# Kernel optimization log

Measured on AMD Instinct MI355X. Metric: run time of the kernel, lower is better.

The kernel has to match this reference:

```python
import jax, jax.numpy as jnp
import numpy as np

C1 = 384  # input channel dim (hardcoded in source)


def setup_inputs() -> dict:
    key = jax.random.key(0)
    kx, kq, kk, kv = jax.random.split(key, 4)
    B, T, C, H = 512, 256, C1, 64
    x = jax.random.normal(kx, (B, T, C), dtype=jnp.float32)
    # nn.Linear(C1, head_size, bias=False) weights, stored as (C, H) for x @ W
    Wq = jax.random.normal(kq, (C, H), dtype=jnp.float32) * (1.0 / np.sqrt(C))
    Wk = jax.random.normal(kk, (C, H), dtype=jnp.float32) * (1.0 / np.sqrt(C))
    Wv = jax.random.normal(kv, (C, H), dtype=jnp.float32) * (1.0 / np.sqrt(C))
    return {"x": x, "Wq": Wq, "Wk": Wk, "Wv": Wv}


def reference(x, Wq, Wk, Wv):
    B, T, C = x.shape
    q = jnp.einsum('btc,ch->bth', x, Wq)  # [B,T,H]
    k = jnp.einsum('btc,ch->bth', x, Wk)
    v = jnp.einsum('btc,ch->bth', x, Wv)
    # NOTE: source MULTIPLIES by C**0.5 (not the usual 1/sqrt(d)) -- faithful.
    scale = jnp.asarray(C, x.dtype) ** 0.5
    wei = jnp.einsum('bth,bsh->bts', q, k) * scale  # [B,T,T]
    causal = jnp.tril(jnp.ones((T, T), dtype=bool))
    wei = jnp.where(causal, wei, -jnp.inf)
    wei = jax.nn.softmax(wei, axis=-1)
    # dropout is identity in eval mode (deterministic reference)
    out = jnp.einsum('bts,bsh->bth', wei, v)  # [B,T,H]
    return out
```

## Files before the change

kernel.cpp:

```cpp
#include <hip/hip_runtime.h>
#include <hip/hip_bf16.h>
#include <math.h>

typedef _Float16 f16x8 __attribute__((ext_vector_type(8)));
typedef _Float16 f16x4 __attribute__((ext_vector_type(4)));
typedef float f32x4 __attribute__((ext_vector_type(4)));

#define MFMA16(a, b, c) __builtin_amdgcn_mfma_f32_16x16x32_f16((a), (b), (c), 0, 0, 0)

typedef __attribute__((address_space(3))) char as3_char;
typedef __attribute__((address_space(1))) const char as1_char;
__device__ __forceinline__ void glds16(const void* g, void* l) {
  __builtin_amdgcn_global_load_lds((as1_char*)g, (as3_char*)l, 16, 0, 0);
}

__global__ __launch_bounds__(256) void wprep_kernel(
    const float* __restrict__ Wq, const float* __restrict__ Wk, const float* __restrict__ Wv,
    _Float16* __restrict__ wstg) {
  int s = blockIdx.x * 256 + threadIdx.x;
  int c0 = s / 1536, s2 = s % 1536;
  int p = s2 / 768, r = (s2 % 768) / 4, gg = s2 & 3;
  int g = gg ^ ((r >> 1) & 3);
  int sel = r >> 6, h = r & 63;
  const float* W = (sel == 0) ? Wq : (sel == 1) ? Wk : Wv;
  f16x8 o;
#pragma unroll
  for (int e = 0; e < 8; ++e) {
    float val = W[(c0 * 32 + g * 8 + e) * 64 + h];
    _Float16 hi = (_Float16)val;
    o[e] = p ? (_Float16)(val - (float)hi) : hi;
  }
  *(f16x8*)&wstg[(size_t)s * 8] = o;
}

__global__ __launch_bounds__(512, 2) void fused_kernel(
    const float* __restrict__ x,
    const _Float16* __restrict__ wstg,
    float* __restrict__ out) {
  __shared__ __align__(16) char smem[156672];
  _Float16* kh = (_Float16*)smem;
  _Float16* kl = (_Float16*)(smem + 36864);
  _Float16* vT = (_Float16*)(smem + 73728);
  char* wbuf0 = smem + 107520;
  char* wbuf1 = smem + 132096;
  _Float16* slc = (_Float16*)(smem + 107520);

  const int tid = threadIdx.x;
  const int wave = tid >> 6, lane = tid & 63;
  const int g = lane >> 4, l16 = lane & 15;
  const int b = blockIdx.x;
  const int rset[2] = {16 * wave, 240 - 16 * wave};
  const float* xb = x + (size_t)b * 98304;
  _Float16* wsl = slc + wave * 2304;

  const float K2 = 28.270933f;
  const float NINF = -__builtin_inff();

  const float* xrow0 = xb + (size_t)(rset[0] + l16) * 384 + g * 8;
  const float* xrow1 = xb + (size_t)(rset[1] + l16) * 384 + g * 8;

  f32x4 qa[2][4] = {}, ka[2][4] = {}, va[2][4] = {};
  float4 buf[3][2][2];

#pragma unroll
  for (int i = 0; i < 3; ++i) {
    int seg0 = wave * 192 + i * 64;
    glds16(wstg + (size_t)(seg0 + lane) * 8, wbuf0 + seg0 * 16);
  }
  __builtin_amdgcn_sched_barrier(0);
#pragma unroll
  for (int p = 0; p < 2; ++p) {
    buf[p][0][0] = *(const float4*)(xrow0 + p * 32);
    buf[p][0][1] = *(const float4*)(xrow0 + p * 32 + 4);
    buf[p][1][0] = *(const float4*)(xrow1 + p * 32);
    buf[p][1][1] = *(const float4*)(xrow1 + p * 32 + 4);
  }
  __builtin_amdgcn_sched_barrier(0);
  asm volatile("s_waitcnt vmcnt(4) lgkmcnt(0)" ::: "memory");
  __builtin_amdgcn_s_barrier();
  __builtin_amdgcn_sched_barrier(0);

#pragma unroll
  for (int c = 0; c < 12; ++c) {
    if (c < 11) {
      char* nb = ((c + 1) & 1) ? wbuf1 : wbuf0;
      const _Float16* src = wstg + (size_t)(c + 1) * 12288;
#pragma unroll
      for (int i = 0; i < 3; ++i) {
        int seg0 = wave * 192 + i * 64;
        glds16(src + (size_t)(seg0 + lane) * 8, nb + seg0 * 16);
      }
    }
    __builtin_amdgcn_sched_barrier(0);
    if (c < 10) {
      buf[(c + 2) % 3][0][0] = *(const float4*)(xrow0 + (c + 2) * 32);
      buf[(c + 2) % 3][0][1] = *(const float4*)(xrow0 + (c + 2) * 32 + 4);
      buf[(c + 2) % 3][1][0] = *(const float4*)(xrow1 + (c + 2) * 32);
      buf[(c + 2) % 3][1][1] = *(const float4*)(xrow1 + (c + 2) * 32 + 4);
    }
    __builtin_amdgcn_sched_barrier(0);

    const char* wb = (c & 1) ? wbuf1 : wbuf0;
    f16x8 ah[2], al[2];
#pragma unroll
    for (int s = 0; s < 2; ++s) {
      float vv[8] = {buf[c % 3][s][0].x, buf[c % 3][s][0].y, buf[c % 3][s][0].z,
                     buf[c % 3][s][0].w, buf[c % 3][s][1].x, buf[c % 3][s][1].y,
                     buf[c % 3][s][1].z, buf[c % 3][s][1].w};
#pragma unroll
      for (int e = 0; e < 8; ++e) {
        _Float16 h = (_Float16)vv[e];
        ah[s][e] = h;
        al[s][e] = (_Float16)(vv[e] - (float)h);
      }
    }
#pragma unroll
    for (int ct = 0; ct < 4; ++ct) {
      const int rq = ct * 16 + l16;
      const int rk = 64 + ct * 16 + l16;
      const int rv = 128 + ct * 16 + l16;
      f16x8 bqh = *(const f16x8*)(wb + (0 * 768 + rq * 4 + (g ^ ((rq >> 1) & 3))) * 16);
      f16x8 bql = *(const f16x8*)(wb + (1 * 768 + rq * 4 + (g ^ ((rq >> 1) & 3))) * 16);
      f16x8 bkh = *(const f16x8*)(wb + (0 * 768 + rk * 4 + (g ^ ((rk >> 1) & 3))) * 16);
      f16x8 bkl = *(const f16x8*)(wb + (1 * 768 + rk * 4 + (g ^ ((rk >> 1) & 3))) * 16);
      f16x8 bvh = *(const f16x8*)(wb + (0 * 768 + rv * 4 + (g ^ ((rv >> 1) & 3))) * 16);
#pragma unroll
      for (int s = 0; s < 2; ++s) {
        qa[s][ct] = MFMA16(ah[s], bqh, qa[s][ct]);
        qa[s][ct] = MFMA16(al[s], bqh, qa[s][ct]);
        qa[s][ct] = MFMA16(ah[s], bql, qa[s][ct]);
        ka[s][ct] = MFMA16(ah[s], bkh, ka[s][ct]);
        ka[s][ct] = MFMA16(al[s], bkh, ka[s][ct]);
        ka[s][ct] = MFMA16(ah[s], bkl, ka[s][ct]);
        va[s][ct] = MFMA16(ah[s], bvh, va[s][ct]);
      }
    }
    if (c < 10) {
      asm volatile("s_waitcnt vmcnt(4) lgkmcnt(0)" ::: "memory");
    } else if (c == 10) {
      asm volatile("s_waitcnt vmcnt(0) lgkmcnt(0)" ::: "memory");
    } else {
      asm volatile("s_waitcnt lgkmcnt(0)" ::: "memory");
    }
    __builtin_amdgcn_s_barrier();
    __builtin_amdgcn_sched_barrier(0);
  }

#pragma unroll
  for (int s = 0; s < 2; ++s) {
    const int rs = rset[s];
#pragma unroll
    for (int ct = 0; ct < 4; ++ct) {
      const int h = ct * 16 + l16;
#pragma unroll
      for (int j = 0; j < 4; ++j) {
        const int row = rs + 4 * g + j;
        float kv = ka[s][ct][j];
        _Float16 khv = (_Float16)kv;
        kh[row * 72 + h] = khv;
        kl[row * 72 + h] = (_Float16)(kv - (float)khv);
        vT[h * 264 + row] = (_Float16)va[s][ct][j];
      }
    }
  }
  __syncthreads();

  f16x8 qhf[2][2], qlf[2][2];
#pragma unroll
  for (int ct = 0; ct < 4; ++ct) {
    const int h = ct * 16 + l16;
#pragma unroll
    for (int j = 0; j < 4; ++j) {
      const int rl = 4 * g + j;
      float qv = qa[0][ct][j];
      _Float16 qh = (_Float16)qv;
      wsl[(rl * 2 + 0) * 72 + h] = qh;
      wsl[(rl * 2 + 1) * 72 + h] = (_Float16)(qv - (float)qh);
    }
  }
  __syncthreads();
#pragma unroll
  for (int ks = 0; ks < 2; ++ks) {
    qhf[0][ks] = *(const f16x8*)&wsl[(l16 * 2 + 0) * 72 + ks * 32 + g * 8];
    qlf[0][ks] = *(const f16x8*)&wsl[(l16 * 2 + 1) * 72 + ks * 32 + g * 8];
  }
  __syncthreads();
#pragma unroll
  for (int ct = 0; ct < 4; ++ct) {
    const int h = ct * 16 + l16;
#pragma unroll
    for (int j = 0; j < 4; ++j) {
      const int rl = 4 * g + j;
      float qv = qa[1][ct][j];
      _Float16 qh = (_Float16)qv;
      wsl[(rl * 2 + 0) * 72 + h] = qh;
      wsl[(rl * 2 + 1) * 72 + h] = (_Float16)(qv - (float)qh);
    }
  }
  __syncthreads();
#pragma unroll
  for (int ks = 0; ks < 2; ++ks) {
    qhf[1][ks] = *(const f16x8*)&wsl[(l16 * 2 + 0) * 72 + ks * 32 + g * 8];
    qlf[1][ks] = *(const f16x8*)&wsl[(l16 * 2 + 1) * 72 + ks * 32 + g * 8];
  }
  asm volatile("s_waitcnt lgkmcnt(0)" ::: "memory");
  __builtin_amdgcn_sched_barrier(0);

  _Float16* psl = wsl;
  float mrun[2] = {NINF, NINF}, srun[2] = {0.f, 0.f};
  f32x4 O[2][4] = {};

  for (int c = 0; c < 4; ++c) {
    const int kb = c * 64;
#pragma unroll
    for (int s = 0; s < 2; ++s) {
      const int rs = rset[s];
      if (kb > rs + 15) continue;
      const int qr = rs + l16;
      f32x4 sa[4] = {};
#pragma unroll
      for (int kt = 0; kt < 4; ++kt) {
        if (kb + 16 * kt > rs + 15) continue;
#pragma unroll
        for (int ks = 0; ks < 2; ++ks) {
          const int ko = (kb + 16 * kt + l16) * 72 + ks * 32 + g * 8;
          f16x8 akh = *(const f16x8*)&kh[ko];
          f16x8 akl = *(const f16x8*)&kl[ko];
          sa[kt] = MFMA16(akh, qhf[s][ks], sa[kt]);
          sa[kt] = MFMA16(akl, qhf[s][ks], sa[kt]);
          sa[kt] = MFMA16(akh, qlf[s][ks], sa[kt]);
        }
      }
      float cm = NINF;
#pragma unroll
      for (int kt = 0; kt < 4; ++kt)
#pragma unroll
        for (int j = 0; j < 4; ++j) {
          const int krow = kb + 16 * kt + 4 * g + j;
          float sv = (krow <= qr) ? sa[kt][j] : NINF;
          sa[kt][j] = sv;
          cm = fmaxf(cm, sv);
        }
      cm = fmaxf(cm, __shfl_xor(cm, 16));
      cm = fmaxf(cm, __shfl_xor(cm, 32));
      const float mn = fmaxf(mrun[s], cm);
      const float scl = exp2f(K2 * (mrun[s] - mn));
      mrun[s] = mn;
      float cs = 0.f;
#pragma unroll
      for (int kt = 0; kt < 4; ++kt)
#pragma unroll
        for (int j = 0; j < 4; ++j) {
          float p = exp2f(K2 * (sa[kt][j] - mn));
          cs += p;
          psl[(s * 16 + l16) * 72 + kt * 16 + 4 * g + j] = (_Float16)p;
        }
      cs += __shfl_xor(cs, 16);
      cs += __shfl_xor(cs, 32);
      srun[s] = srun[s] * scl + cs;
#pragma unroll
      for (int ht = 0; ht < 4; ++ht) O[s][ht] *= scl;
      asm volatile("s_waitcnt lgkmcnt(0)" ::: "memory");
      __builtin_amdgcn_sched_barrier(0);
#pragma unroll
      for (int ks2 = 0; ks2 < 2; ++ks2) {
        f16x8 bp = *(const f16x8*)&psl[(s * 16 + l16) * 72 + ks2 * 32 + g * 8];
#pragma unroll
        for (int ht = 0; ht < 4; ++ht) {
          f16x8 av = *(const f16x8*)&vT[(ht * 16 + l16) * 264 + kb + ks2 * 32 + g * 8];
          O[s][ht] = MFMA16(av, bp, O[s][ht]);
        }
      }
    }
  }

#pragma unroll
  for (int s = 0; s < 2; ++s) {
    const int qr = rset[s] + l16;
    const float inv = 1.0f / srun[s];
#pragma unroll
    for (int ht = 0; ht < 4; ++ht) {
      f32x4 r = O[s][ht] * inv;
      *(f32x4*)&out[((size_t)b * 256 + qr) * 64 + ht * 16 + 4 * g] = r;
    }
  }
}

extern "C" void kernel_launch(void* const* d_in, const int* in_sizes, int n_in,
                              void* d_out, int out_size, void* d_ws, size_t ws_size,
                              hipStream_t stream) {
  const float* x  = (const float*)d_in[0];
  const float* Wq = (const float*)d_in[1];
  const float* Wk = (const float*)d_in[2];
  const float* Wv = (const float*)d_in[3];

  _Float16* wstg = (_Float16*)d_ws;

  wprep_kernel<<<72, 256, 0, stream>>>(Wq, Wk, Wv, wstg);
  fused_kernel<<<512, 512, 0, stream>>>(x, wstg, (float*)d_out);
}
```

Measured before the change: 86.00 us.

## Fuse both query row-sets per key chunk, use packed f16 converts and setprio

The attention loop now processes both 16-row query sets together inside each key chunk. Each K and V fragment loaded from LDS is reused for two MFMA chains, and the two softmax updates run before a single shared PV stage. The hi/lo fp16 split of x uses packed round-toward-zero conversions (cvt_pkrtz) in place of per-element casts. s_setprio is raised around MFMA bursts. This cuts LDS reads and exposes more independent MFMA work, at the cost of more live registers and a rounding mode change on the high part, which the low-part residual compensates for.

```diff
diff --git a/kernel.cpp b/kernel.cpp
--- a/kernel.cpp
+++ b/kernel.cpp
@@ -4,6 +4,8 @@
 
 typedef _Float16 f16x8 __attribute__((ext_vector_type(8)));
 typedef _Float16 f16x4 __attribute__((ext_vector_type(4)));
+typedef _Float16 f16x2 __attribute__((ext_vector_type(2)));
+typedef __fp16 fp16x2 __attribute__((ext_vector_type(2)));
 typedef float f32x4 __attribute__((ext_vector_type(4)));
 
 #define MFMA16(a, b, c) __builtin_amdgcn_mfma_f32_16x16x32_f16((a), (b), (c), 0, 0, 0)
@@ -12,6 +14,13 @@
 typedef __attribute__((address_space(1))) const char as1_char;
 __device__ __forceinline__ void glds16(const void* g, void* l) {
   __builtin_amdgcn_global_load_lds((as1_char*)g, (as3_char*)l, 16, 0, 0);
+}
+
+union F16x8u { f16x8 v; f16x2 h[4]; };
+
+__device__ __forceinline__ f16x2 pkrtz(float a, float b) {
+  fp16x2 r = __builtin_amdgcn_cvt_pkrtz(a, b);
+  return __builtin_bit_cast(f16x2, r);
 }
 
 __global__ __launch_bounds__(256) void wprep_kernel(
@@ -107,12 +116,16 @@
       float vv[8] = {buf[c % 3][s][0].x, buf[c % 3][s][0].y, buf[c % 3][s][0].z,
                      buf[c % 3][s][0].w, buf[c % 3][s][1].x, buf[c % 3][s][1].y,
                      buf[c % 3][s][1].z, buf[c % 3][s][1].w};
-#pragma unroll
-      for (int e = 0; e < 8; ++e) {
-        _Float16 h = (_Float16)vv[e];
-        ah[s][e] = h;
-        al[s][e] = (_Float16)(vv[e] - (float)h);
-      }
+      F16x8u uh, ul;
+#pragma unroll
+      for (int k2 = 0; k2 < 4; ++k2) {
+        float a = vv[2 * k2], bb = vv[2 * k2 + 1];
+        f16x2 hp = pkrtz(a, bb);
+        uh.h[k2] = hp;
+        ul.h[k2] = pkrtz(a - (float)hp[0], bb - (float)hp[1]);
+      }
+      ah[s] = uh.v;
+      al[s] = ul.v;
     }
 #pragma unroll
     for (int ct = 0; ct < 4; ++ct) {
@@ -124,6 +137,7 @@
       f16x8 bkh = *(const f16x8*)(wb + (0 * 768 + rk * 4 + (g ^ ((rk >> 1) & 3))) * 16);
       f16x8 bkl = *(const f16x8*)(wb + (1 * 768 + rk * 4 + (g ^ ((rk >> 1) & 3))) * 16);
       f16x8 bvh = *(const f16x8*)(wb + (0 * 768 + rv * 4 + (g ^ ((rv >> 1) & 3))) * 16);
+      __builtin_amdgcn_s_setprio(1);
 #pragma unroll
       for (int s = 0; s < 2; ++s) {
         qa[s][ct] = MFMA16(ah[s], bqh, qa[s][ct]);
@@ -134,6 +148,7 @@
         ka[s][ct] = MFMA16(ah[s], bkl, ka[s][ct]);
         va[s][ct] = MFMA16(ah[s], bvh, va[s][ct]);
       }
+      __builtin_amdgcn_s_setprio(0);
     }
     if (c < 10) {
       asm volatile("s_waitcnt vmcnt(4) lgkmcnt(0)" ::: "memory");
@@ -209,67 +224,116 @@
   _Float16* psl = wsl;
   float mrun[2] = {NINF, NINF}, srun[2] = {0.f, 0.f};
   f32x4 O[2][4] = {};
+  const int rs0 = rset[0], rs1 = rset[1];
+  const int qr0 = rs0 + l16, qr1 = rs1 + l16;
 
   for (int c = 0; c < 4; ++c) {
     const int kb = c * 64;
-#pragma unroll
-    for (int s = 0; s < 2; ++s) {
-      const int rs = rset[s];
-      if (kb > rs + 15) continue;
-      const int qr = rs + l16;
-      f32x4 sa[4] = {};
-#pragma unroll
-      for (int kt = 0; kt < 4; ++kt) {
-        if (kb + 16 * kt > rs + 15) continue;
-#pragma unroll
-        for (int ks = 0; ks < 2; ++ks) {
-          const int ko = (kb + 16 * kt + l16) * 72 + ks * 32 + g * 8;
-          f16x8 akh = *(const f16x8*)&kh[ko];
-          f16x8 akl = *(const f16x8*)&kl[ko];
-          sa[kt] = MFMA16(akh, qhf[s][ks], sa[kt]);
-          sa[kt] = MFMA16(akl, qhf[s][ks], sa[kt]);
-          sa[kt] = MFMA16(akh, qlf[s][ks], sa[kt]);
-        }
-      }
+    const bool a0 = (kb <= rs0 + 15);
+    const bool a1 = (kb <= rs1 + 15);
+    if (!a0 && !a1) continue;
+    f32x4 s0[4] = {}, s1[4] = {};
+#pragma unroll
+    for (int kt = 0; kt < 4; ++kt) {
+      const int kr = kb + 16 * kt;
+      const bool t0 = a0 && (kr <= rs0 + 15);
+      const bool t1 = a1 && (kr <= rs1 + 15);
+      if (!t0 && !t1) continue;
+#pragma unroll
+      for (int ks = 0; ks < 2; ++ks) {
+        const int ko = (kr + l16) * 72 + ks * 32 + g * 8;
+        f16x8 akh = *(const f16x8*)&kh[ko];
+        f16x8 akl = *(const f16x8*)&kl[ko];
+        __builtin_amdgcn_s_setprio(1);
+        if (t0) {
+          s0[kt] = MFMA16(akh, qhf[0][ks], s0[kt]);
+          s0[kt] = MFMA16(akl, qhf[0][ks], s0[kt]);
+          s0[kt] = MFMA16(akh, qlf[0][ks], s0[kt]);
+        }
+        if (t1) {
+          s1[kt] = MFMA16(akh, qhf[1][ks], s1[kt]);
+          s1[kt] = MFMA16(akl, qhf[1][ks], s1[kt]);
+          s1[kt] = MFMA16(akh, qlf[1][ks], s1[kt]);
+        }
+        __builtin_amdgcn_s_setprio(0);
+      }
+    }
+    if (a0) {
       float cm = NINF;
 #pragma unroll
       for (int kt = 0; kt < 4; ++kt)
 #pragma unroll
         for (int j = 0; j < 4; ++j) {
           const int krow = kb + 16 * kt + 4 * g + j;
-          float sv = (krow <= qr) ? sa[kt][j] : NINF;
-          sa[kt][j] = sv;
+          float sv = (krow <= qr0) ? s0[kt][j] : NINF;
+          s0[kt][j] = sv;
           cm = fmaxf(cm, sv);
         }
       cm = fmaxf(cm, __shfl_xor(cm, 16));
       cm = fmaxf(cm, __shfl_xor(cm, 32));
-      const float mn = fmaxf(mrun[s], cm);
-      const float scl = exp2f(K2 * (mrun[s] - mn));
-      mrun[s] = mn;
+      const float mn = fmaxf(mrun[0], cm);
+      const float scl = exp2f(K2 * (mrun[0] - mn));
+      mrun[0] = mn;
       float cs = 0.f;
 #pragma unroll
       for (int kt = 0; kt < 4; ++kt)
 #pragma unroll
         for (int j = 0; j < 4; ++j) {
-          float p = exp2f(K2 * (sa[kt][j] - mn));
+          float p = exp2f(K2 * (s0[kt][j] - mn));
           cs += p;
-          psl[(s * 16 + l16) * 72 + kt * 16 + 4 * g + j] = (_Float16)p;
+          psl[l16 * 72 + kt * 16 + 4 * g + j] = (_Float16)p;
         }
       cs += __shfl_xor(cs, 16);
       cs += __shfl_xor(cs, 32);
-      srun[s] = srun[s] * scl + cs;
-#pragma unroll
-      for (int ht = 0; ht < 4; ++ht) O[s][ht] *= scl;
-      asm volatile("s_waitcnt lgkmcnt(0)" ::: "memory");
-      __builtin_amdgcn_sched_barrier(0);
-#pragma unroll
-      for (int ks2 = 0; ks2 < 2; ++ks2) {
-        f16x8 bp = *(const f16x8*)&psl[(s * 16 + l16) * 72 + ks2 * 32 + g * 8];
-#pragma unroll
-        for (int ht = 0; ht < 4; ++ht) {
-          f16x8 av = *(const f16x8*)&vT[(ht * 16 + l16) * 264 + kb + ks2 * 32 + g * 8];
-          O[s][ht] = MFMA16(av, bp, O[s][ht]);
-        }
+      srun[0] = srun[0] * scl + cs;
+#pragma unroll
+      for (int ht = 0; ht < 4; ++ht) O[0][ht] *= scl;
+    }
+    if (a1) {
+      float cm = NINF;
+#pragma unroll
+      for (int kt = 0; kt < 4; ++kt)
+#pragma unroll
+        for (int j = 0; j < 4; ++j) {
+          const int krow = kb + 16 * kt + 4 * g + j;
+          float sv = (krow <= qr1) ? s1[kt][j] : NINF;
+          s1[kt][j] = sv;
+          cm = fmaxf(cm, sv);
+        }
+      cm = fmaxf(cm, __shfl_xor(cm, 16));
+      cm = fmaxf(cm, __shfl_xor(cm, 32));
+      const float mn = fmaxf(mrun[1], cm);
+      const float scl = exp2f(K2 * (mrun[1] - mn));
+      mrun[1] = mn;
+      float cs = 0.f;
+#pragma unroll
+      for (int kt = 0; kt < 4; ++kt)
+#pragma unroll
+        for (int j = 0; j < 4; ++j) {
+          float p = exp2f(K2 * (s1[kt][j] - mn));
+          cs += p;
+          psl[(16 + l16) * 72 + kt * 16 + 4 * g + j] = (_Float16)p;
+        }
+      cs += __shfl_xor(cs, 16);
+      cs += __shfl_xor(cs, 32);
+      srun[1] = srun[1] * scl + cs;
+#pragma unroll
+      for (int ht = 0; ht < 4; ++ht) O[1][ht] *= scl;
+    }
+    asm volatile("s_waitcnt lgkmcnt(0)" ::: "memory");
+    __builtin_amdgcn_sched_barrier(0);
+#pragma unroll
+    for (int ks2 = 0; ks2 < 2; ++ks2) {
+      f16x8 bp0 = {}, bp1 = {};
+      if (a0) bp0 = *(const f16x8*)&psl[l16 * 72 + ks2 * 32 + g * 8];
+      if (a1) bp1 = *(const f16x8*)&psl[(16 + l16) * 72 + ks2 * 32 + g * 8];
+#pragma unroll
+      for (int ht = 0; ht < 4; ++ht) {
+        f16x8 av = *(const f16x8*)&vT[(ht * 16 + l16) * 264 + kb + ks2 * 32 + g * 8];
+        __builtin_amdgcn_s_setprio(1);
+        if (a0) O[0][ht] = MFMA16(av, bp0, O[0][ht]);
+        if (a1) O[1][ht] = MFMA16(av, bp1, O[1][ht]);
+        __builtin_amdgcn_s_setprio(0);
       }
     }
   }
```

After: 83.63 us. 1.03x faster.

## Use 16 waves per block with one 16-row query tile per wave

Applied to the files above, without the earlier changes.

The fused attention kernel moves from 8 waves, each owning two row tiles (a low and a mirrored high tile for causal balance), to 16 waves per block, each owning one 16-row tile. The aim is to double the waves available per block for latency hiding. Only 12 waves issue weight loads into LDS, Q staging is done in two rounds, and MFMA sections are wrapped in s_setprio. Conversion to fp16 hi/lo now uses packed cvt_pkrtz, which rounds toward zero and can shift precision slightly. Costs: the causal load balance from paired tiles is lost, so later waves do much more work than early ones, and register pressure under launch bounds of 1024 may force spills.

```diff
diff --git a/kernel.cpp b/kernel.cpp
--- a/kernel.cpp
+++ b/kernel.cpp
@@ -4,6 +4,8 @@
 
 typedef _Float16 f16x8 __attribute__((ext_vector_type(8)));
 typedef _Float16 f16x4 __attribute__((ext_vector_type(4)));
+typedef _Float16 f16x2 __attribute__((ext_vector_type(2)));
+typedef __fp16 fp16x2 __attribute__((ext_vector_type(2)));
 typedef float f32x4 __attribute__((ext_vector_type(4)));
 
 #define MFMA16(a, b, c) __builtin_amdgcn_mfma_f32_16x16x32_f16((a), (b), (c), 0, 0, 0)
@@ -12,6 +14,13 @@
 typedef __attribute__((address_space(1))) const char as1_char;
 __device__ __forceinline__ void glds16(const void* g, void* l) {
   __builtin_amdgcn_global_load_lds((as1_char*)g, (as3_char*)l, 16, 0, 0);
+}
+
+union F16x8u { f16x8 v; f16x2 h[4]; };
+
+__device__ __forceinline__ f16x2 pkrtz(float a, float b) {
+  fp16x2 r = __builtin_amdgcn_cvt_pkrtz(a, b);
+  return __builtin_bit_cast(f16x2, r);
 }
 
 __global__ __launch_bounds__(256) void wprep_kernel(
@@ -33,7 +42,7 @@
   *(f16x8*)&wstg[(size_t)s * 8] = o;
 }
 
-__global__ __launch_bounds__(512, 2) void fused_kernel(
+__global__ __launch_bounds__(1024) void fused_kernel(
     const float* __restrict__ x,
     const _Float16* __restrict__ wstg,
     float* __restrict__ out) {
@@ -49,70 +58,70 @@
   const int wave = tid >> 6, lane = tid & 63;
   const int g = lane >> 4, l16 = lane & 15;
   const int b = blockIdx.x;
-  const int rset[2] = {16 * wave, 240 - 16 * wave};
+  const int rs = 16 * wave;
+  const int qr = rs + l16;
   const float* xb = x + (size_t)b * 98304;
-  _Float16* wsl = slc + wave * 2304;
 
   const float K2 = 28.270933f;
   const float NINF = -__builtin_inff();
 
-  const float* xrow0 = xb + (size_t)(rset[0] + l16) * 384 + g * 8;
-  const float* xrow1 = xb + (size_t)(rset[1] + l16) * 384 + g * 8;
-
-  f32x4 qa[2][4] = {}, ka[2][4] = {}, va[2][4] = {};
-  float4 buf[3][2][2];
-
-#pragma unroll
-  for (int i = 0; i < 3; ++i) {
-    int seg0 = wave * 192 + i * 64;
-    glds16(wstg + (size_t)(seg0 + lane) * 8, wbuf0 + seg0 * 16);
+  const float* xrow = xb + (size_t)qr * 384 + g * 8;
+
+  f32x4 qa[4] = {}, ka[4] = {}, va[4] = {};
+  float4 buf[3][2];
+
+  if (wave < 12) {
+#pragma unroll
+    for (int i = 0; i < 2; ++i) {
+      int seg0 = wave * 128 + i * 64;
+      glds16(wstg + (size_t)(seg0 + lane) * 8, wbuf0 + seg0 * 16);
+    }
   }
   __builtin_amdgcn_sched_barrier(0);
 #pragma unroll
   for (int p = 0; p < 2; ++p) {
-    buf[p][0][0] = *(const float4*)(xrow0 + p * 32);
-    buf[p][0][1] = *(const float4*)(xrow0 + p * 32 + 4);
-    buf[p][1][0] = *(const float4*)(xrow1 + p * 32);
-    buf[p][1][1] = *(const float4*)(xrow1 + p * 32 + 4);
-  }
-  __builtin_amdgcn_sched_barrier(0);
-  asm volatile("s_waitcnt vmcnt(4) lgkmcnt(0)" ::: "memory");
+    buf[p][0] = *(const float4*)(xrow + p * 32);
+    buf[p][1] = *(const float4*)(xrow + p * 32 + 4);
+  }
+  __builtin_amdgcn_sched_barrier(0);
+  asm volatile("s_waitcnt vmcnt(2) lgkmcnt(0)" ::: "memory");
   __builtin_amdgcn_s_barrier();
   __builtin_amdgcn_sched_barrier(0);
 
 #pragma unroll
   for (int c = 0; c < 12; ++c) {
-    if (c < 11) {
+    if (wave < 12 && c < 11) {
       char* nb = ((c + 1) & 1) ? wbuf1 : wbuf0;
       const _Float16* src = wstg + (size_t)(c + 1) * 12288;
 #pragma unroll
-      for (int i = 0; i < 3; ++i) {
-        int seg0 = wave * 192 + i * 64;
+      for (int i = 0; i < 2; ++i) {
+        int seg0 = wave * 128 + i * 64;
         glds16(src + (size_t)(seg0 + lane) * 8, nb + seg0 * 16);
       }
     }
     __builtin_amdgcn_sched_barrier(0);
     if (c < 10) {
-      buf[(c + 2) % 3][0][0] = *(const float4*)(xrow0 + (c + 2) * 32);
-      buf[(c + 2) % 3][0][1] = *(const float4*)(xrow0 + (c + 2) * 32 + 4);
-      buf[(c + 2) % 3][1][0] = *(const float4*)(xrow1 + (c + 2) * 32);
-      buf[(c + 2) % 3][1][1] = *(const float4*)(xrow1 + (c + 2) * 32 + 4);
+      buf[(c + 2) % 3][0] = *(const float4*)(xrow + (c + 2) * 32);
+      buf[(c + 2) % 3][1] = *(const float4*)(xrow + (c + 2) * 32 + 4);
     }
     __builtin_amdgcn_sched_barrier(0);
 
     const char* wb = (c & 1) ? wbuf1 : wbuf0;
-    f16x8 ah[2], al[2];
-#pragma unroll
-    for (int s = 0; s < 2; ++s) {
-      float vv[8] = {buf[c % 3][s][0].x, buf[c % 3][s][0].y, buf[c % 3][s][0].z,
-                     buf[c % 3][s][0].w, buf[c % 3][s][1].x, buf[c % 3][s][1].y,
-                     buf[c % 3][s][1].z, buf[c % 3][s][1].w};
-#pragma unroll
-      for (int e = 0; e < 8; ++e) {
-        _Float16 h = (_Float16)vv[e];
-        ah[s][e] = h;
-        al[s][e] = (_Float16)(vv[e] - (float)h);
-      }
+    f16x8 ah, al;
+    {
+      float vv[8] = {buf[c % 3][0].x, buf[c % 3][0].y, buf[c % 3][0].z,
+                     buf[c % 3][0].w, buf[c % 3][1].x, buf[c % 3][1].y,
+                     buf[c % 3][1].z, buf[c % 3][1].w};
+      F16x8u uh, ul;
+#pragma unroll
+      for (int k2 = 0; k2 < 4; ++k2) {
+        float a = vv[2 * k2], bb = vv[2 * k2 + 1];
+        f16x2 hp = pkrtz(a, bb);
+        uh.h[k2] = hp;
+        ul.h[k2] = pkrtz(a - (float)hp[0], bb - (float)hp[1]);
+      }
+      ah = uh.v;
+      al = ul.v;
     }
 #pragma unroll
     for (int ct = 0; ct < 4; ++ct) {
@@ -124,19 +133,18 @@
       f16x8 bkh = *(const f16x8*)(wb + (0 * 768 + rk * 4 + (g ^ ((rk >> 1) & 3))) * 16);
       f16x8 bkl = *(const f16x8*)(wb + (1 * 768 + rk * 4 + (g ^ ((rk >> 1) & 3))) * 16);
       f16x8 bvh = *(const f16x8*)(wb + (0 * 768 + rv * 4 + (g ^ ((rv >> 1) & 3))) * 16);
-#pragma unroll
-      for (int s = 0; s < 2; ++s) {
-        qa[s][ct] = MFMA16(ah[s], bqh, qa[s][ct]);
-        qa[s][ct] = MFMA16(al[s], bqh, qa[s][ct]);
-        qa[s][ct] = MFMA16(ah[s], bql, qa[s][ct]);
-        ka[s][ct] = MFMA16(ah[s], bkh, ka[s][ct]);
-        ka[s][ct] = MFMA16(al[s], bkh, ka[s][ct]);
-        ka[s][ct] = MFMA16(ah[s], bkl, ka[s][ct]);
-        va[s][ct] = MFMA16(ah[s], bvh, va[s][ct]);
-      }
+      __builtin_amdgcn_s_setprio(1);
+      qa[ct] = MFMA16(ah, bqh, qa[ct]);
+      qa[ct] = MFMA16(al, bqh, qa[ct]);
+      qa[ct] = MFMA16(ah, bql, qa[ct]);
+      ka[ct] = MFMA16(ah, bkh, ka[ct]);
+      ka[ct] = MFMA16(al, bkh, ka[ct]);
+      ka[ct] = MFMA16(ah, bkl, ka[ct]);
+      va[ct] = MFMA16(ah, bvh, va[ct]);
+      __builtin_amdgcn_s_setprio(0);
     }
     if (c < 10) {
-      asm volatile("s_waitcnt vmcnt(4) lgkmcnt(0)" ::: "memory");
+      asm volatile("s_waitcnt vmcnt(2) lgkmcnt(0)" ::: "memory");
     } else if (c == 10) {
       asm volatile("s_waitcnt vmcnt(0) lgkmcnt(0)" ::: "memory");
     } else {
@@ -147,142 +155,124 @@
   }
 
 #pragma unroll
-  for (int s = 0; s < 2; ++s) {
-    const int rs = rset[s];
-#pragma unroll
-    for (int ct = 0; ct < 4; ++ct) {
-      const int h = ct * 16 + l16;
-#pragma unroll
-      for (int j = 0; j < 4; ++j) {
-        const int row = rs + 4 * g + j;
-        float kv = ka[s][ct][j];
-        _Float16 khv = (_Float16)kv;
-        kh[row * 72 + h] = khv;
-        kl[row * 72 + h] = (_Float16)(kv - (float)khv);
-        vT[h * 264 + row] = (_Float16)va[s][ct][j];
-      }
-    }
-  }
-  __syncthreads();
-
-  f16x8 qhf[2][2], qlf[2][2];
-#pragma unroll
   for (int ct = 0; ct < 4; ++ct) {
     const int h = ct * 16 + l16;
 #pragma unroll
     for (int j = 0; j < 4; ++j) {
-      const int rl = 4 * g + j;
-      float qv = qa[0][ct][j];
-      _Float16 qh = (_Float16)qv;
-      wsl[(rl * 2 + 0) * 72 + h] = qh;
-      wsl[(rl * 2 + 1) * 72 + h] = (_Float16)(qv - (float)qh);
+      const int row = rs + 4 * g + j;
+      float kv = ka[ct][j];
+      _Float16 khv = (_Float16)kv;
+      kh[row * 72 + h] = khv;
+      kl[row * 72 + h] = (_Float16)(kv - (float)khv);
+      vT[h * 264 + row] = (_Float16)va[ct][j];
     }
   }
   __syncthreads();
-#pragma unroll
-  for (int ks = 0; ks < 2; ++ks) {
-    qhf[0][ks] = *(const f16x8*)&wsl[(l16 * 2 + 0) * 72 + ks * 32 + g * 8];
-    qlf[0][ks] = *(const f16x8*)&wsl[(l16 * 2 + 1) * 72 + ks * 32 + g * 8];
-  }
-  __syncthreads();
-#pragma unroll
-  for (int ct = 0; ct < 4; ++ct) {
-    const int h = ct * 16 + l16;
-#pragma unroll
-    for (int j = 0; j < 4; ++j) {
-      const int rl = 4 * g + j;
-      float qv = qa[1][ct][j];
-      _Float16 qh = (_Float16)qv;
-      wsl[(rl * 2 + 0) * 72 + h] = qh;
-      wsl[(rl * 2 + 1) * 72 + h] = (_Float16)(qv - (float)qh);
-    }
-  }
-  __syncthreads();
-#pragma unroll
-  for (int ks = 0; ks < 2; ++ks) {
-    qhf[1][ks] = *(const f16x8*)&wsl[(l16 * 2 + 0) * 72 + ks * 32 + g * 8];
-    qlf[1][ks] = *(const f16x8*)&wsl[(l16 * 2 + 1) * 72 + ks * 32 + g * 8];
+
+  _Float16* myq = slc + (wave & 7) * 2304;
+  f16x8 qhf[2], qlf[2];
+#pragma unroll
+  for (int rnd = 0; rnd < 2; ++rnd) {
+    if ((wave >> 3) == rnd) {
+#pragma unroll
+      for (int ct = 0; ct < 4; ++ct) {
+        const int h = ct * 16 + l16;
+#pragma unroll
+        for (int j = 0; j < 4; ++j) {
+          const int rl = 4 * g + j;
+          float qv = qa[ct][j];
+          _Float16 qh = (_Float16)qv;
+          myq[(rl * 2 + 0) * 72 + h] = qh;
+          myq[(rl * 2 + 1) * 72 + h] = (_Float16)(qv - (float)qh);
+        }
+      }
+    }
+    __syncthreads();
+    if ((wave >> 3) == rnd) {
+#pragma unroll
+      for (int ks = 0; ks < 2; ++ks) {
+        qhf[ks] = *(const f16x8*)&myq[(l16 * 2 + 0) * 72 + ks * 32 + g * 8];
+        qlf[ks] = *(const f16x8*)&myq[(l16 * 2 + 1) * 72 + ks * 32 + g * 8];
+      }
+    }
+    __syncthreads();
   }
   asm volatile("s_waitcnt lgkmcnt(0)" ::: "memory");
   __builtin_amdgcn_sched_barrier(0);
 
-  _Float16* psl = wsl;
-  float mrun[2] = {NINF, NINF}, srun[2] = {0.f, 0.f};
-  f32x4 O[2][4] = {};
+  _Float16* psl = slc + wave * 1152;
+  float mrun = NINF, srun = 0.f;
+  f32x4 O[4] = {};
 
   for (int c = 0; c < 4; ++c) {
     const int kb = c * 64;
-#pragma unroll
-    for (int s = 0; s < 2; ++s) {
-      const int rs = rset[s];
-      if (kb > rs + 15) continue;
-      const int qr = rs + l16;
-      f32x4 sa[4] = {};
-#pragma unroll
-      for (int kt = 0; kt < 4; ++kt) {
-        if (kb + 16 * kt > rs + 15) continue;
-#pragma unroll
-        for (int ks = 0; ks < 2; ++ks) {
-          const int ko = (kb + 16 * kt + l16) * 72 + ks * 32 + g * 8;
-          f16x8 akh = *(const f16x8*)&kh[ko];
-          f16x8 akl = *(const f16x8*)&kl[ko];
-          sa[kt] = MFMA16(akh, qhf[s][ks], sa[kt]);
-          sa[kt] = MFMA16(akl, qhf[s][ks], sa[kt]);
-          sa[kt] = MFMA16(akh, qlf[s][ks], sa[kt]);
-        }
-      }
-      float cm = NINF;
-#pragma unroll
-      for (int kt = 0; kt < 4; ++kt)
-#pragma unroll
-        for (int j = 0; j < 4; ++j) {
-          const int krow = kb + 16 * kt + 4 * g + j;
-          float sv = (krow <= qr) ? sa[kt][j] : NINF;
-          sa[kt][j] = sv;
-          cm = fmaxf(cm, sv);
-        }
-      cm = fmaxf(cm, __shfl_xor(cm, 16));
-      cm = fmaxf(cm, __shfl_xor(cm, 32));
-      const float mn = fmaxf(mrun[s], cm);
-      const float scl = exp2f(K2 * (mrun[s] - mn));
-      mrun[s] = mn;
-      float cs = 0.f;
-#pragma unroll
-      for (int kt = 0; kt < 4; ++kt)
-#pragma unroll
-        for (int j = 0; j < 4; ++j) {
-          float p = exp2f(K2 * (sa[kt][j] - mn));
-          cs += p;
-          psl[(s * 16 + l16) * 72 + kt * 16 + 4 * g + j] = (_Float16)p;
-        }
-      cs += __shfl_xor(cs, 16);
-      cs += __shfl_xor(cs, 32);
-      srun[s] = srun[s] * scl + cs;
-#pragma unroll
-      for (int ht = 0; ht < 4; ++ht) O[s][ht] *= scl;
-      asm volatile("s_waitcnt lgkmcnt(0)" ::: "memory");
-      __builtin_amdgcn_sched_barrier(0);
-#pragma unroll
-      for (int ks2 = 0; ks2 < 2; ++ks2) {
-        f16x8 bp = *(const f16x8*)&psl[(s * 16 + l16) * 72 + ks2 * 32 + g * 8];
-#pragma unroll
-        for (int ht = 0; ht < 4; ++ht) {
-          f16x8 av = *(const f16x8*)&vT[(ht * 16 + l16) * 264 + kb + ks2 * 32 + g * 8];
-          O[s][ht] = MFMA16(av, bp, O[s][ht]);
-        }
-      }
-    }
-  }
-
-#pragma unroll
-  for (int s = 0; s < 2; ++s) {
-    const int qr = rset[s] + l16;
-    const float inv = 1.0f / srun[s];
-#pragma unroll
-    for (int ht = 0; ht < 4; ++ht) {
-      f32x4 r = O[s][ht] * inv;
-      *(f32x4*)&out[((size_t)b * 256 + qr) * 64 + ht * 16 + 4 * g] = r;
-    }
+    if (kb > rs + 15) continue;
+    f32x4 sa[4] = {};
+#pragma unroll
+    for (int kt = 0; kt < 4; ++kt) {
+      const int kr = kb + 16 * kt;
+      if (kr > rs + 15) continue;
+#pragma unroll
+      for (int ks = 0; ks < 2; ++ks) {
+        const int ko = (kr + l16) * 72 + ks * 32 + g * 8;
+        f16x8 akh = *(const f16x8*)&kh[ko];
+        f16x8 akl = *(const f16x8*)&kl[ko];
+        __builtin_amdgcn_s_setprio(1);
+        sa[kt] = MFMA16(akh, qhf[ks], sa[kt]);
+        sa[kt] = MFMA16(akl, qhf[ks], sa[kt]);
+        sa[kt] = MFMA16(akh, qlf[ks], sa[kt]);
+        __builtin_amdgcn_s_setprio(0);
+      }
+    }
+    float cm = NINF;
+#pragma unroll
+    for (int kt = 0; kt < 4; ++kt)
+#pragma unroll
+      for (int j = 0; j < 4; ++j) {
+        const int krow = kb + 16 * kt + 4 * g + j;
+        float sv = (krow <= qr) ? sa[kt][j] : NINF;
+        sa[kt][j] = sv;
+        cm = fmaxf(cm, sv);
+      }
+    cm = fmaxf(cm, __shfl_xor(cm, 16));
+    cm = fmaxf(cm, __shfl_xor(cm, 32));
+    const float mn = fmaxf(mrun, cm);
+    const float scl = exp2f(K2 * (mrun - mn));
+    mrun = mn;
+    float cs = 0.f;
+#pragma unroll
+    for (int kt = 0; kt < 4; ++kt)
+#pragma unroll
+      for (int j = 0; j < 4; ++j) {
+        float p = exp2f(K2 * (sa[kt][j] - mn));
+        cs += p;
+        psl[l16 * 72 + kt * 16 + 4 * g + j] = (_Float16)p;
+      }
+    cs += __shfl_xor(cs, 16);
+    cs += __shfl_xor(cs, 32);
+    srun = srun * scl + cs;
+#pragma unroll
+    for (int ht = 0; ht < 4; ++ht) O[ht] *= scl;
+    asm volatile("s_waitcnt lgkmcnt(0)" ::: "memory");
+    __builtin_amdgcn_sched_barrier(0);
+#pragma unroll
+    for (int ks2 = 0; ks2 < 2; ++ks2) {
+      f16x8 bp = *(const f16x8*)&psl[l16 * 72 + ks2 * 32 + g * 8];
+#pragma unroll
+      for (int ht = 0; ht < 4; ++ht) {
+        f16x8 av = *(const f16x8*)&vT[(ht * 16 + l16) * 264 + kb + ks2 * 32 + g * 8];
+        __builtin_amdgcn_s_setprio(1);
+        O[ht] = MFMA16(av, bp, O[ht]);
+        __builtin_amdgcn_s_setprio(0);
+      }
+    }
+  }
+
+  const float inv = 1.0f / srun;
+#pragma unroll
+  for (int ht = 0; ht < 4; ++ht) {
+    f32x4 r = O[ht] * inv;
+    *(f32x4*)&out[((size_t)b * 256 + qr) * 64 + ht * 16 + 4 * g] = r;
   }
 }
 
@@ -297,5 +287,5 @@
   _Float16* wstg = (_Float16*)d_ws;
 
   wprep_kernel<<<72, 256, 0, stream>>>(Wq, Wk, Wv, wstg);
-  fused_kernel<<<512, 512, 0, stream>>>(x, wstg, (float*)d_out);
-}
+  fused_kernel<<<512, 1024, 0, stream>>>(x, wstg, (float*)d_out);
+}
```

After: 81.63 us. 1.05x faster.
